# Optimization experiments

Measured on AMD Instinct MI355X. Metric: run time of the kernel, lower is better.

Reference implementation:

```python
import jax, jax.numpy as jnp
import numpy as np

BS = 15
NA = BS * BS
NOISE_SCALE = 2.0
TEMP = 0.03
VALUE_NOISE = 200.0

def _build_windows():
    # all length-5 windows in the 4 directions of a 15x15 board (572 total)
    wins = []
    for dr, dc in ((0, 1), (1, 0), (1, 1), (1, -1)):
        for r in range(BS):
            for c in range(BS):
                er, ec = r + 4 * dr, c + 4 * dc
                if 0 <= er < BS and 0 <= ec < BS:
                    wins.append([(r + k * dr) * BS + (c + k * dc) for k in range(5)])
    return np.asarray(wins, dtype=np.int32)

_WIN = _build_windows()                      # [572, 5] flat cell indices
_NW = _WIN.shape[0]
_Mnp = np.zeros((NA, _NW), dtype=np.float32)  # membership: cell i in window w
for w in range(_NW):
    _Mnp[_WIN[w], w] = 1.0
WIN_CELLS = jnp.asarray(_WIN)
MEMBER = jnp.asarray(_Mnp)                   # [225, 572]
WEIGHTS = jnp.asarray([0.0, 5.0, 50.0, 500.0, 5000.0, 100000.0], dtype=jnp.float32)

def _window_score(pc, oc):
    # matches _eval_board's per-window scoring table
    sp = jnp.where((oc == 0) & (pc > 0), WEIGHTS[jnp.minimum(pc, 5)], 0.0)
    so = jnp.where((pc == 0) & (oc > 0), WEIGHTS[jnp.minimum(oc, 5)], 0.0)
    return sp - so

def setup_inputs() -> dict:
    key = jax.random.key(0)
    k1, k2, k3, k4 = jax.random.split(key, 4)
    B = 8192
    boards = jax.random.randint(k1, (B, NA), 0, 3, dtype=jnp.int32)
    current_player = jax.random.randint(k2, (B,), 1, 3, dtype=jnp.int32)
    policy_noise = jax.random.normal(k3, (B, NA), dtype=jnp.float32)
    value_noise = jax.random.normal(k4, (B,), dtype=jnp.float32)
    return {"boards": boards, "current_player": current_player,
            "policy_noise": policy_noise, "value_noise": value_noise}

def reference(boards, current_player, policy_noise, value_noise):
    player = current_player[:, None, None]           # [B,1,1]
    opp = 3 - player
    cells = boards[:, WIN_CELLS]                      # [B, 572, 5]
    pc0 = jnp.sum(cells == player, axis=-1)           # [B, 572] player stones per window
    oc0 = jnp.sum(cells == opp, axis=-1)              # [B, 572] opponent stones per window
    s0 = _window_score(pc0, oc0)                      # base per-window score
    base = jnp.sum(s0, axis=-1)                       # [B] = _eval_board(board, player)
    # placing a player stone in an empty cell adds +1 to pc of every window containing it
    d = _window_score(pc0 + 1, oc0) - s0              # [B, 572]
    delta = jnp.einsum('bw,aw->ba', d, MEMBER)        # [B, 225]
    win_w = ((pc0 == 4) & (oc0 == 0)).astype(jnp.float32)
    win = jnp.einsum('bw,aw->ba', win_w, MEMBER) > 0  # [B, 225]
    empty = boards == 0
    logits = jnp.where(empty, jnp.where(win, 1e5, base[:, None] + delta), -1e6)
    valid = logits > -1e5                             # matches `logits > -100000.0`
    n = jnp.sum(valid, axis=-1).astype(jnp.float32)
    nsafe = jnp.maximum(n, 1.0)
    mean = jnp.sum(jnp.where(valid, logits, 0.0), axis=-1) / nsafe
    var = jnp.sum(jnp.where(valid, (logits - mean[:, None]) ** 2, 0.0), axis=-1) / nsafe
    std = jnp.maximum(1.0, jnp.sqrt(var))             # population std, floored at 1
    logits = logits + jnp.where(valid & (n[:, None] > 0),
                                policy_noise * NOISE_SCALE * std[:, None], 0.0)
    policy = jax.nn.softmax(logits * TEMP, axis=-1)   # [B, 225]
    value = jnp.clip(jnp.tanh((base + value_noise * VALUE_NOISE) / 3000.0), -0.95, 0.95)[:, None]
    return policy, value
```

## Files before the change

kernel.cpp:

```cpp
#include <hip/hip_runtime.h>
#include <math.h>

#define BSZ 15
#define NA  225
typedef unsigned long long u64;

__device__ __forceinline__ float wtab(int n) {
    return n == 1 ? 5.f : n == 2 ? 50.f : n == 3 ? 500.f : n == 4 ? 5000.f : 100000.f;
}
__device__ __forceinline__ float wredSum(float v) {
    #pragma unroll
    for (int off = 32; off; off >>= 1) v += __shfl_xor(v, off, 64);
    return v;
}
__device__ __forceinline__ float wredMax(float v) {
    #pragma unroll
    for (int off = 32; off; off >>= 1) v = fmaxf(v, __shfl_xor(v, off, 64));
    return v;
}

struct Masks { u64 P0, P1, P2, P3, O0, O1, O2, O3; };

template<int DIV, int CEXTRA, bool HAS64>
__device__ __forceinline__ void extractWin(int u, const Masks& M, u64 wmask,
                                           int& pc, int& oc, int& idx)
{
    const int r = u / DIV;
    const int c = u % DIV + CEXTRA;
    idx = r * BSZ + c;
    const int q = idx >> 6, sh = idx & 63;
    const u64 Plo = (q & 2) ? ((q & 1) ? M.P3 : M.P2) : ((q & 1) ? M.P1 : M.P0);
    const u64 Phi = (q & 2) ? ((q & 1) ? 0ULL : M.P3) : ((q & 1) ? M.P2 : M.P1);
    const u64 Olo = (q & 2) ? ((q & 1) ? M.O3 : M.O2) : ((q & 1) ? M.O1 : M.O0);
    const u64 Ohi = (q & 2) ? ((q & 1) ? 0ULL : M.O3) : ((q & 1) ? M.O2 : M.O1);
    const u64 xP = (Plo >> sh) | ((Phi << (63 - sh)) << 1);
    const u64 xO = (Olo >> sh) | ((Ohi << (63 - sh)) << 1);
    pc = __popcll(xP & wmask);
    oc = __popcll(xO & wmask);
    if (HAS64) {
        pc += (int)((Phi >> sh) & 1ULL);
        oc += (int)((Ohi >> sh) & 1ULL);
    }
}

template<int STEP>
__device__ __forceinline__ void scoreWin(bool act, int pc, int oc, int idx,
                                         float* __restrict__ bD,
                                         float* __restrict__ bW,
                                         float& baseLocal)
{
    if (!act) return;
    const bool z_oc = (oc == 0), z_pc = (pc == 0);
    const float s0 = z_oc ? (z_pc ? 0.f : wtab(pc)) : (z_pc ? -wtab(oc) : 0.f);
    const float d  = (z_oc ? wtab(pc + 1) : 0.f) - s0;
    baseLocal += s0;
    if (d != 0.f) {
        #pragma unroll
        for (int k = 0; k < 5; ++k) atomicAdd(&bD[idx + k * STEP], d);
    }
    if (pc == 4 && z_oc) {
        #pragma unroll
        for (int k = 0; k < 5; ++k) bW[idx + k * STEP] = 1.f;
    }
}

__global__ __launch_bounds__(256, 4) void heur_kernel(
    const int* __restrict__ boards, const int* __restrict__ cur,
    const float* __restrict__ pnoise, const float* __restrict__ vnoise,
    float* __restrict__ out, int B)
{
    const int wid  = threadIdx.x >> 6;
    const int lane = threadIdx.x & 63;
    const int b    = blockIdx.x * 4 + wid;

    __shared__ float sDelta[4][NA];
    __shared__ float sWin[4][NA];

    if (b >= B) return;

    float* __restrict__ bD = sDelta[wid];
    float* __restrict__ bW = sWin[wid];

    const int player = cur[b];
    const int opp    = 3 - player;
    const int* __restrict__ gb = boards + (size_t)b * NA;

    const int v0 = gb[lane];
    const int v1 = gb[lane + 64];
    const int v2 = gb[lane + 128];
    const int v3 = (lane + 192 < NA) ? gb[lane + 192] : -1;

    const float* __restrict__ pn = pnoise + (size_t)b * NA;
    float pnv[4];
    pnv[0] = pn[lane];
    pnv[1] = pn[lane + 64];
    pnv[2] = pn[lane + 128];
    pnv[3] = (lane + 192 < NA) ? pn[lane + 192] : 0.f;
    const float vnb = vnoise[b];

    Masks M;
    M.P0 = __ballot(v0 == player); M.O0 = __ballot(v0 == opp);
    M.P1 = __ballot(v1 == player); M.O1 = __ballot(v1 == opp);
    M.P2 = __ballot(v2 == player); M.O2 = __ballot(v2 == opp);
    M.P3 = __ballot(v3 == player); M.O3 = __ballot(v3 == opp);

    bD[lane] = 0.f;       bW[lane] = 0.f;
    bD[lane + 64] = 0.f;  bW[lane + 64] = 0.f;
    bD[lane + 128] = 0.f; bW[lane + 128] = 0.f;
    if (lane + 192 < NA) { bD[lane + 192] = 0.f; bW[lane + 192] = 0.f; }
    __threadfence_block();

    const u64 MH = 0x1FULL;
    const u64 MV = 0x1000200040008001ULL;
    const u64 MD = 0x0001000100010001ULL;
    const u64 MA = 0x0100040010004001ULL;

    int pcS[10], ocS[10], ixS[10];
    const bool a2 = lane < 37, a5 = lane < 37, a7 = lane < 57, a9 = lane < 57;
    extractWin<11, 0, false>(lane,                 M, MH, pcS[0], ocS[0], ixS[0]);
    extractWin<11, 0, false>(lane + 64,            M, MH, pcS[1], ocS[1], ixS[1]);
    extractWin<11, 0, false>(min(lane + 128, 164), M, MH, pcS[2], ocS[2], ixS[2]);
    extractWin<15, 0, false>(lane,                 M, MV, pcS[3], ocS[3], ixS[3]);
    extractWin<15, 0, false>(lane + 64,            M, MV, pcS[4], ocS[4], ixS[4]);
    extractWin<15, 0, false>(min(lane + 128, 164), M, MV, pcS[5], ocS[5], ixS[5]);
    extractWin<11, 0, true >(lane,                 M, MD, pcS[6], ocS[6], ixS[6]);
    extractWin<11, 0, true >(min(lane + 64, 120),  M, MD, pcS[7], ocS[7], ixS[7]);
    extractWin<11, 4, false>(lane,                 M, MA, pcS[8], ocS[8], ixS[8]);
    extractWin<11, 4, false>(min(lane + 64, 120),  M, MA, pcS[9], ocS[9], ixS[9]);

    float baseLocal = 0.f;
    scoreWin<1> (true, pcS[0], ocS[0], ixS[0], bD, bW, baseLocal);
    scoreWin<1> (true, pcS[1], ocS[1], ixS[1], bD, bW, baseLocal);
    scoreWin<1> (a2,   pcS[2], ocS[2], ixS[2], bD, bW, baseLocal);
    scoreWin<15>(true, pcS[3], ocS[3], ixS[3], bD, bW, baseLocal);
    scoreWin<15>(true, pcS[4], ocS[4], ixS[4], bD, bW, baseLocal);
    scoreWin<15>(a5,   pcS[5], ocS[5], ixS[5], bD, bW, baseLocal);
    scoreWin<16>(true, pcS[6], ocS[6], ixS[6], bD, bW, baseLocal);
    scoreWin<16>(a7,   pcS[7], ocS[7], ixS[7], bD, bW, baseLocal);
    scoreWin<14>(true, pcS[8], ocS[8], ixS[8], bD, bW, baseLocal);
    scoreWin<14>(a9,   pcS[9], ocS[9], ixS[9], bD, bW, baseLocal);

    __threadfence_block();

    const float base = wredSum(baseLocal);

    const u64 C0 = M.P0 | M.O0, C1 = M.P1 | M.O1, C2 = M.P2 | M.O2, C3 = M.P3 | M.O3;

    float logitv[4];
    float nLoc = 0.f, sLoc = 0.f;
    #pragma unroll
    for (int j = 0; j < 4; ++j) {
        const int c = lane + 64 * j;
        float lg = -1000000.f;
        if (c < NA) {
            const u64 Cj = j == 0 ? C0 : j == 1 ? C1 : j == 2 ? C2 : C3;
            const bool isEmpty = ((Cj >> lane) & 1ULL) == 0ULL;
            if (isEmpty) lg = (bW[c] > 0.f) ? 100000.f : base + bD[c];
        }
        logitv[j] = lg;
        if (c < NA && lg > -100000.f) { nLoc += 1.f; sLoc += lg; }
    }
    #pragma unroll
    for (int off = 32; off; off >>= 1) {
        nLoc += __shfl_xor(nLoc, off, 64);
        sLoc += __shfl_xor(sLoc, off, 64);
    }
    const float nsafe = fmaxf(nLoc, 1.f);
    const float mean  = sLoc / nsafe;

    float vLoc = 0.f;
    #pragma unroll
    for (int j = 0; j < 4; ++j) {
        const int c = lane + 64 * j;
        if (c < NA && logitv[j] > -100000.f) {
            const float dv = logitv[j] - mean;
            vLoc += dv * dv;
        }
    }
    const float var  = wredSum(vLoc) / nsafe;
    const float std_ = fmaxf(1.f, sqrtf(var));
    const float nsc  = 2.0f * std_;
    const bool  anyValid = nLoc > 0.f;

    #pragma unroll
    for (int j = 0; j < 4; ++j) {
        const int c = lane + 64 * j;
        if (c < NA && logitv[j] > -100000.f && anyValid)
            logitv[j] += pnv[j] * nsc;
    }

    float xs[4];
    float mLoc = -INFINITY;
    #pragma unroll
    for (int j = 0; j < 4; ++j) {
        const int c = lane + 64 * j;
        xs[j] = logitv[j] * 0.03f;
        if (c < NA) mLoc = fmaxf(mLoc, xs[j]);
    }
    const float m = wredMax(mLoc);

    float ev[4];
    float eLoc = 0.f;
    #pragma unroll
    for (int j = 0; j < 4; ++j) {
        const int c = lane + 64 * j;
        ev[j] = (c < NA) ? __expf(xs[j] - m) : 0.f;
        eLoc += ev[j];
    }
    const float inv = 1.f / wredSum(eLoc);

    float* __restrict__ po = out + (size_t)b * NA;
    #pragma unroll
    for (int j = 0; j < 4; ++j) {
        const int c = lane + 64 * j;
        if (c < NA) po[c] = ev[j] * inv;
    }

    if (lane == 0) {
        float v = tanhf((base + vnb * 200.0f) / 3000.0f);
        v = fminf(0.95f, fmaxf(-0.95f, v));
        out[(size_t)B * NA + b] = v;
    }
}

extern "C" void kernel_launch(void* const* d_in, const int* in_sizes, int n_in,
                              void* d_out, int out_size, void* d_ws, size_t ws_size,
                              hipStream_t stream) {
    const int*   boards = (const int*)d_in[0];
    const int*   cur    = (const int*)d_in[1];
    const float* pn     = (const float*)d_in[2];
    const float* vn     = (const float*)d_in[3];
    float*       outp   = (float*)d_out;
    const int B = in_sizes[1];

    const int grid = (B + 3) / 4;
    heur_kernel<<<grid, 256, 0, stream>>>(boards, cur, pn, vn, outp, B);
}
```

Baseline: 110.6 us.

## Split fused kernel into window-scoring and softmax kernels via workspace

Splits the single kernel into two: one computes per-cell logits and the base score and writes them to a global workspace, and a second reads them back along with the noise to do normalisation, noise injection, softmax and value output. The likely intent is to lower register pressure and raise occupancy in each part. The cost is an extra global round trip of about B*225 floats plus a second kernel launch. The lane-bound masks a5/a9 are merged into a2/a7, which have identical values.

```diff
diff --git a/kernel.cpp b/kernel.cpp
--- a/kernel.cpp
+++ b/kernel.cpp
@@ -64,10 +64,9 @@
     }
 }
 
-__global__ __launch_bounds__(256, 4) void heur_kernel(
+__global__ __launch_bounds__(256, 4) void win_kernel(
     const int* __restrict__ boards, const int* __restrict__ cur,
-    const float* __restrict__ pnoise, const float* __restrict__ vnoise,
-    float* __restrict__ out, int B)
+    float* __restrict__ ws, int B)
 {
     const int wid  = threadIdx.x >> 6;
     const int lane = threadIdx.x & 63;
@@ -89,14 +88,6 @@
     const int v1 = gb[lane + 64];
     const int v2 = gb[lane + 128];
     const int v3 = (lane + 192 < NA) ? gb[lane + 192] : -1;
-
-    const float* __restrict__ pn = pnoise + (size_t)b * NA;
-    float pnv[4];
-    pnv[0] = pn[lane];
-    pnv[1] = pn[lane + 64];
-    pnv[2] = pn[lane + 128];
-    pnv[3] = (lane + 192 < NA) ? pn[lane + 192] : 0.f;
-    const float vnb = vnoise[b];
 
     Masks M;
     M.P0 = __ballot(v0 == player); M.O0 = __ballot(v0 == opp);
@@ -116,7 +107,7 @@
     const u64 MA = 0x0100040010004001ULL;
 
     int pcS[10], ocS[10], ixS[10];
-    const bool a2 = lane < 37, a5 = lane < 37, a7 = lane < 57, a9 = lane < 57;
+    const bool a2 = lane < 37, a7 = lane < 57;
     extractWin<11, 0, false>(lane,                 M, MH, pcS[0], ocS[0], ixS[0]);
     extractWin<11, 0, false>(lane + 64,            M, MH, pcS[1], ocS[1], ixS[1]);
     extractWin<11, 0, false>(min(lane + 128, 164), M, MH, pcS[2], ocS[2], ixS[2]);
@@ -134,11 +125,11 @@
     scoreWin<1> (a2,   pcS[2], ocS[2], ixS[2], bD, bW, baseLocal);
     scoreWin<15>(true, pcS[3], ocS[3], ixS[3], bD, bW, baseLocal);
     scoreWin<15>(true, pcS[4], ocS[4], ixS[4], bD, bW, baseLocal);
-    scoreWin<15>(a5,   pcS[5], ocS[5], ixS[5], bD, bW, baseLocal);
+    scoreWin<15>(a2,   pcS[5], ocS[5], ixS[5], bD, bW, baseLocal);
     scoreWin<16>(true, pcS[6], ocS[6], ixS[6], bD, bW, baseLocal);
     scoreWin<16>(a7,   pcS[7], ocS[7], ixS[7], bD, bW, baseLocal);
     scoreWin<14>(true, pcS[8], ocS[8], ixS[8], bD, bW, baseLocal);
-    scoreWin<14>(a9,   pcS[9], ocS[9], ixS[9], bD, bW, baseLocal);
+    scoreWin<14>(a7,   pcS[9], ocS[9], ixS[9], bD, bW, baseLocal);
 
     __threadfence_block();
 
@@ -146,19 +137,48 @@
 
     const u64 C0 = M.P0 | M.O0, C1 = M.P1 | M.O1, C2 = M.P2 | M.O2, C3 = M.P3 | M.O3;
 
-    float logitv[4];
-    float nLoc = 0.f, sLoc = 0.f;
-    #pragma unroll
-    for (int j = 0; j < 4; ++j) {
-        const int c = lane + 64 * j;
-        float lg = -1000000.f;
+    float* __restrict__ pl = ws + (size_t)b * NA;
+    #pragma unroll
+    for (int j = 0; j < 4; ++j) {
+        const int c = lane + 64 * j;
         if (c < NA) {
             const u64 Cj = j == 0 ? C0 : j == 1 ? C1 : j == 2 ? C2 : C3;
             const bool isEmpty = ((Cj >> lane) & 1ULL) == 0ULL;
+            float lg = -1000000.f;
             if (isEmpty) lg = (bW[c] > 0.f) ? 100000.f : base + bD[c];
+            pl[c] = lg;
         }
-        logitv[j] = lg;
-        if (c < NA && lg > -100000.f) { nLoc += 1.f; sLoc += lg; }
+    }
+    if (lane == 0) ws[(size_t)B * NA + b] = base;
+}
+
+__global__ __launch_bounds__(256, 4) void sm_kernel(
+    const float* __restrict__ ws, const float* __restrict__ pnoise,
+    const float* __restrict__ vnoise, float* __restrict__ out, int B)
+{
+    const int wid  = threadIdx.x >> 6;
+    const int lane = threadIdx.x & 63;
+    const int b    = blockIdx.x * 4 + wid;
+    if (b >= B) return;
+
+    const float* __restrict__ pl = ws + (size_t)b * NA;
+    const float* __restrict__ pn = pnoise + (size_t)b * NA;
+
+    float lg[4], pnv[4];
+    #pragma unroll
+    for (int j = 0; j < 4; ++j) {
+        const int c = lane + 64 * j;
+        lg[j]  = (c < NA) ? pl[c] : -1000000.f;
+        pnv[j] = (c < NA) ? pn[c] : 0.f;
+    }
+    const float vnb  = vnoise[b];
+    const float base = ws[(size_t)B * NA + b];
+
+    float nLoc = 0.f, sLoc = 0.f;
+    #pragma unroll
+    for (int j = 0; j < 4; ++j) {
+        const int c = lane + 64 * j;
+        if (c < NA && lg[j] > -100000.f) { nLoc += 1.f; sLoc += lg[j]; }
     }
     #pragma unroll
     for (int off = 32; off; off >>= 1) {
@@ -172,8 +192,8 @@
     #pragma unroll
     for (int j = 0; j < 4; ++j) {
         const int c = lane + 64 * j;
-        if (c < NA && logitv[j] > -100000.f) {
-            const float dv = logitv[j] - mean;
+        if (c < NA && lg[j] > -100000.f) {
+            const float dv = lg[j] - mean;
             vLoc += dv * dv;
         }
     }
@@ -185,8 +205,8 @@
     #pragma unroll
     for (int j = 0; j < 4; ++j) {
         const int c = lane + 64 * j;
-        if (c < NA && logitv[j] > -100000.f && anyValid)
-            logitv[j] += pnv[j] * nsc;
+        if (c < NA && lg[j] > -100000.f && anyValid)
+            lg[j] += pnv[j] * nsc;
     }
 
     float xs[4];
@@ -194,7 +214,7 @@
     #pragma unroll
     for (int j = 0; j < 4; ++j) {
         const int c = lane + 64 * j;
-        xs[j] = logitv[j] * 0.03f;
+        xs[j] = lg[j] * 0.03f;
         if (c < NA) mLoc = fmaxf(mLoc, xs[j]);
     }
     const float m = wredMax(mLoc);
@@ -231,8 +251,10 @@
     const float* pn     = (const float*)d_in[2];
     const float* vn     = (const float*)d_in[3];
     float*       outp   = (float*)d_out;
+    float*       wsf    = (float*)d_ws;
     const int B = in_sizes[1];
 
     const int grid = (B + 3) / 4;
-    heur_kernel<<<grid, 256, 0, stream>>>(boards, cur, pn, vn, outp, B);
-}
+    win_kernel<<<grid, 256, 0, stream>>>(boards, cur, wsf, B);
+    sm_kernel <<<grid, 256, 0, stream>>>(wsf, pn, vn, outp, B);
+}
```

Result: slower. 116.9 us (+5.8%).

## Replace atomic scatter of window deltas with per-cell gather from window array

Applied to the files above, without the earlier changes.

Each window now stores its score delta once into a shared per-window array instead of atomically adding it into five cell slots. Each cell then gathers the contributing windows across the four directions. A winning window is detected by its delta value equalling 95000, which removes the separate win array. This drops the LDS atomics and zero-initialisation, at the cost of more shared-memory reads and index arithmetic per cell.

```diff
diff --git a/kernel.cpp b/kernel.cpp
--- a/kernel.cpp
+++ b/kernel.cpp
@@ -23,11 +23,11 @@
 
 template<int DIV, int CEXTRA, bool HAS64>
 __device__ __forceinline__ void extractWin(int u, const Masks& M, u64 wmask,
-                                           int& pc, int& oc, int& idx)
+                                           int& pc, int& oc)
 {
     const int r = u / DIV;
     const int c = u % DIV + CEXTRA;
-    idx = r * BSZ + c;
+    const int idx = r * BSZ + c;
     const int q = idx >> 6, sh = idx & 63;
     const u64 Plo = (q & 2) ? ((q & 1) ? M.P3 : M.P2) : ((q & 1) ? M.P1 : M.P0);
     const u64 Phi = (q & 2) ? ((q & 1) ? 0ULL : M.P3) : ((q & 1) ? M.P2 : M.P1);
@@ -43,25 +43,10 @@
     }
 }
 
-template<int STEP>
-__device__ __forceinline__ void scoreWin(bool act, int pc, int oc, int idx,
-                                         float* __restrict__ bD,
-                                         float* __restrict__ bW,
-                                         float& baseLocal)
-{
-    if (!act) return;
+__device__ __forceinline__ void scoreD(int pc, int oc, float& s0, float& d) {
     const bool z_oc = (oc == 0), z_pc = (pc == 0);
-    const float s0 = z_oc ? (z_pc ? 0.f : wtab(pc)) : (z_pc ? -wtab(oc) : 0.f);
-    const float d  = (z_oc ? wtab(pc + 1) : 0.f) - s0;
-    baseLocal += s0;
-    if (d != 0.f) {
-        #pragma unroll
-        for (int k = 0; k < 5; ++k) atomicAdd(&bD[idx + k * STEP], d);
-    }
-    if (pc == 4 && z_oc) {
-        #pragma unroll
-        for (int k = 0; k < 5; ++k) bW[idx + k * STEP] = 1.f;
-    }
+    s0 = z_oc ? (z_pc ? 0.f : wtab(pc)) : (z_pc ? -wtab(oc) : 0.f);
+    d  = (z_oc ? wtab(pc + 1) : 0.f) - s0;
 }
 
 __global__ __launch_bounds__(256, 4) void heur_kernel(
@@ -73,13 +58,11 @@
     const int lane = threadIdx.x & 63;
     const int b    = blockIdx.x * 4 + wid;
 
-    __shared__ float sDelta[4][NA];
-    __shared__ float sWin[4][NA];
+    __shared__ float sDW[4][572];
 
     if (b >= B) return;
 
-    float* __restrict__ bD = sDelta[wid];
-    float* __restrict__ bW = sWin[wid];
+    float* __restrict__ dw = sDW[wid];
 
     const int player = cur[b];
     const int opp    = 3 - player;
@@ -104,41 +87,42 @@
     M.P2 = __ballot(v2 == player); M.O2 = __ballot(v2 == opp);
     M.P3 = __ballot(v3 == player); M.O3 = __ballot(v3 == opp);
 
-    bD[lane] = 0.f;       bW[lane] = 0.f;
-    bD[lane + 64] = 0.f;  bW[lane + 64] = 0.f;
-    bD[lane + 128] = 0.f; bW[lane + 128] = 0.f;
-    if (lane + 192 < NA) { bD[lane + 192] = 0.f; bW[lane + 192] = 0.f; }
-    __threadfence_block();
-
     const u64 MH = 0x1FULL;
     const u64 MV = 0x1000200040008001ULL;
     const u64 MD = 0x0001000100010001ULL;
     const u64 MA = 0x0100040010004001ULL;
 
-    int pcS[10], ocS[10], ixS[10];
-    const bool a2 = lane < 37, a5 = lane < 37, a7 = lane < 57, a9 = lane < 57;
-    extractWin<11, 0, false>(lane,                 M, MH, pcS[0], ocS[0], ixS[0]);
-    extractWin<11, 0, false>(lane + 64,            M, MH, pcS[1], ocS[1], ixS[1]);
-    extractWin<11, 0, false>(min(lane + 128, 164), M, MH, pcS[2], ocS[2], ixS[2]);
-    extractWin<15, 0, false>(lane,                 M, MV, pcS[3], ocS[3], ixS[3]);
-    extractWin<15, 0, false>(lane + 64,            M, MV, pcS[4], ocS[4], ixS[4]);
-    extractWin<15, 0, false>(min(lane + 128, 164), M, MV, pcS[5], ocS[5], ixS[5]);
-    extractWin<11, 0, true >(lane,                 M, MD, pcS[6], ocS[6], ixS[6]);
-    extractWin<11, 0, true >(min(lane + 64, 120),  M, MD, pcS[7], ocS[7], ixS[7]);
-    extractWin<11, 4, false>(lane,                 M, MA, pcS[8], ocS[8], ixS[8]);
-    extractWin<11, 4, false>(min(lane + 64, 120),  M, MA, pcS[9], ocS[9], ixS[9]);
+    int pcS[10], ocS[10];
+    const bool a2 = lane < 37, a7 = lane < 57;
+    extractWin<11, 0, false>(lane,                 M, MH, pcS[0], ocS[0]);
+    extractWin<11, 0, false>(lane + 64,            M, MH, pcS[1], ocS[1]);
+    extractWin<11, 0, false>(min(lane + 128, 164), M, MH, pcS[2], ocS[2]);
+    extractWin<15, 0, false>(lane,                 M, MV, pcS[3], ocS[3]);
+    extractWin<15, 0, false>(lane + 64,            M, MV, pcS[4], ocS[4]);
+    extractWin<15, 0, false>(min(lane + 128, 164), M, MV, pcS[5], ocS[5]);
+    extractWin<11, 0, true >(lane,                 M, MD, pcS[6], ocS[6]);
+    extractWin<11, 0, true >(min(lane + 64, 120),  M, MD, pcS[7], ocS[7]);
+    extractWin<11, 4, false>(lane,                 M, MA, pcS[8], ocS[8]);
+    extractWin<11, 4, false>(min(lane + 64, 120),  M, MA, pcS[9], ocS[9]);
 
     float baseLocal = 0.f;
-    scoreWin<1> (true, pcS[0], ocS[0], ixS[0], bD, bW, baseLocal);
-    scoreWin<1> (true, pcS[1], ocS[1], ixS[1], bD, bW, baseLocal);
-    scoreWin<1> (a2,   pcS[2], ocS[2], ixS[2], bD, bW, baseLocal);
-    scoreWin<15>(true, pcS[3], ocS[3], ixS[3], bD, bW, baseLocal);
-    scoreWin<15>(true, pcS[4], ocS[4], ixS[4], bD, bW, baseLocal);
-    scoreWin<15>(a5,   pcS[5], ocS[5], ixS[5], bD, bW, baseLocal);
-    scoreWin<16>(true, pcS[6], ocS[6], ixS[6], bD, bW, baseLocal);
-    scoreWin<16>(a7,   pcS[7], ocS[7], ixS[7], bD, bW, baseLocal);
-    scoreWin<14>(true, pcS[8], ocS[8], ixS[8], bD, bW, baseLocal);
-    scoreWin<14>(a9,   pcS[9], ocS[9], ixS[9], bD, bW, baseLocal);
+    float s0v[10], dv[10];
+    #pragma unroll
+    for (int t = 0; t < 10; ++t) scoreD(pcS[t], ocS[t], s0v[t], dv[t]);
+    const bool act[10] = {true, true, a2, true, true, a2, true, a7, true, a7};
+    #pragma unroll
+    for (int t = 0; t < 10; ++t) if (act[t]) baseLocal += s0v[t];
+
+    dw[lane]             = dv[0];
+    dw[lane + 64]        = dv[1];
+    if (a2) dw[lane + 128] = dv[2];
+    dw[165 + lane]       = dv[3];
+    dw[165 + lane + 64]  = dv[4];
+    if (a2) dw[165 + lane + 128] = dv[5];
+    dw[330 + lane]       = dv[6];
+    if (a7) dw[330 + lane + 64]  = dv[7];
+    dw[451 + lane]       = dv[8];
+    if (a7) dw[451 + lane + 64]  = dv[9];
 
     __threadfence_block();
 
@@ -150,16 +134,33 @@
     float nLoc = 0.f, sLoc = 0.f;
     #pragma unroll
     for (int j = 0; j < 4; ++j) {
-        const int c = lane + 64 * j;
+        const int cl = lane + 64 * j;
         float lg = -1000000.f;
-        if (c < NA) {
+        if (cl < NA) {
+            const int r = cl / BSZ, c = cl % BSZ;
+            float acc = 0.f;
+            bool  wf  = false;
+            #pragma unroll
+            for (int k = 0; k < 5; ++k) {
+                const int wr = r - k;
+                const int wcH = c - k;
+                const int wcA = c + k - 4;
+                const bool vR = (unsigned)wr  < 11u;
+                const bool vH = (unsigned)wcH < 11u;
+                const bool vA = (unsigned)wcA < 11u;
+                if (vH)        { const float v = dw[r * 11 + wcH];          acc += v; wf |= (v == 95000.f); }
+                if (vR)        { const float v = dw[165 + wr * 15 + c];     acc += v; wf |= (v == 95000.f); }
+                if (vR && vH)  { const float v = dw[330 + wr * 11 + wcH];   acc += v; wf |= (v == 95000.f); }
+                if (vR && vA)  { const float v = dw[451 + wr * 11 + wcA];   acc += v; wf |= (v == 95000.f); }
+            }
             const u64 Cj = j == 0 ? C0 : j == 1 ? C1 : j == 2 ? C2 : C3;
             const bool isEmpty = ((Cj >> lane) & 1ULL) == 0ULL;
-            if (isEmpty) lg = (bW[c] > 0.f) ? 100000.f : base + bD[c];
+            if (isEmpty) lg = wf ? 100000.f : base + acc;
         }
         logitv[j] = lg;
-        if (c < NA && lg > -100000.f) { nLoc += 1.f; sLoc += lg; }
-    }
+        if (cl < NA && lg > -100000.f) { nLoc += 1.f; sLoc += lg; }
+    }
+
     #pragma unroll
     for (int off = 32; off; off >>= 1) {
         nLoc += __shfl_xor(nLoc, off, 64);
@@ -171,10 +172,10 @@
     float vLoc = 0.f;
     #pragma unroll
     for (int j = 0; j < 4; ++j) {
-        const int c = lane + 64 * j;
-        if (c < NA && logitv[j] > -100000.f) {
-            const float dv = logitv[j] - mean;
-            vLoc += dv * dv;
+        const int cl = lane + 64 * j;
+        if (cl < NA && logitv[j] > -100000.f) {
+            const float dvv = logitv[j] - mean;
+            vLoc += dvv * dvv;
         }
     }
     const float var  = wredSum(vLoc) / nsafe;
@@ -184,8 +185,8 @@
 
     #pragma unroll
     for (int j = 0; j < 4; ++j) {
-        const int c = lane + 64 * j;
-        if (c < NA && logitv[j] > -100000.f && anyValid)
+        const int cl = lane + 64 * j;
+        if (cl < NA && logitv[j] > -100000.f && anyValid)
             logitv[j] += pnv[j] * nsc;
     }
 
@@ -193,9 +194,9 @@
     float mLoc = -INFINITY;
     #pragma unroll
     for (int j = 0; j < 4; ++j) {
-        const int c = lane + 64 * j;
+        const int cl = lane + 64 * j;
         xs[j] = logitv[j] * 0.03f;
-        if (c < NA) mLoc = fmaxf(mLoc, xs[j]);
+        if (cl < NA) mLoc = fmaxf(mLoc, xs[j]);
     }
     const float m = wredMax(mLoc);
 
@@ -203,8 +204,8 @@
     float eLoc = 0.f;
     #pragma unroll
     for (int j = 0; j < 4; ++j) {
-        const int c = lane + 64 * j;
-        ev[j] = (c < NA) ? __expf(xs[j] - m) : 0.f;
+        const int cl = lane + 64 * j;
+        ev[j] = (cl < NA) ? __expf(xs[j] - m) : 0.f;
         eLoc += ev[j];
     }
     const float inv = 1.f / wredSum(eLoc);
@@ -212,8 +213,8 @@
     float* __restrict__ po = out + (size_t)b * NA;
     #pragma unroll
     for (int j = 0; j < 4; ++j) {
-        const int c = lane + 64 * j;
-        if (c < NA) po[c] = ev[j] * inv;
+        const int cl = lane + 64 * j;
+        if (cl < NA) po[cl] = ev[j] * inv;
     }
 
     if (lane == 0) {
```

Measured after the change: 95.57 us. 13.6% less time.
